# Kernel optimization log

Hardware: AMD Instinct MI355X
Metric: run time of the kernel (lower is better)

Reference implementation:

```python
import jax, jax.numpy as jnp
import numpy as np

B, T, C, H = 2, 2048, 1024, 16
D = C // H  # head_dim = 64

def setup_inputs() -> dict:
    key = jax.random.key(0)
    ks = jax.random.split(key, 5)
    x = jax.random.normal(ks[0], (B, T, C), dtype=jnp.float32)
    Wqkv = jax.random.normal(ks[1], (C, 3 * C), dtype=jnp.float32) * 0.02
    bqkv = jnp.zeros((3 * C,), dtype=jnp.float32)
    Wout = jax.random.normal(ks[2], (C, C), dtype=jnp.float32) * 0.02
    bout = jnp.zeros((C,), dtype=jnp.float32)
    return {"x": x, "Wqkv": Wqkv, "bqkv": bqkv, "Wout": Wout, "bout": bout}

def reference(x, Wqkv, bqkv, Wout, bout):
    Bb, Tt, Cc = x.shape
    qkv = x @ Wqkv + bqkv                       # [B,T,3C]
    qkv = qkv.reshape(Bb, Tt, 3, H, D)
    qkv = jnp.transpose(qkv, (2, 0, 3, 1, 4))   # [3,B,H,T,D]
    q, k, v = qkv[0], qkv[1], qkv[2]
    scale = 1.0 / np.sqrt(D).astype(np.float32)
    scores = jnp.einsum('bhqd,bhkd->bhqk', q, k) * scale  # [B,H,T,T]
    causal = jnp.tril(jnp.ones((Tt, Tt), dtype=bool))
    scores = jnp.where(causal[None, None, :, :], scores, jnp.float32(-jnp.inf))
    attn = jax.nn.softmax(scores, axis=-1)
    out = jnp.einsum('bhqk,bhkd->bhqd', attn, v)          # [B,H,T,D]
    out = jnp.transpose(out, (0, 2, 1, 3)).reshape(Bb, Tt, Cc)
    return out @ Wout + bout
```

## Files before the change

kernel.cpp:

```cpp
#include <hip/hip_runtime.h>

#define Bc 2
#define Tc 2048
#define Cc 1024
#define Hc 16
#define Dc 64
#define Mtot (Bc*Tc)
#define Kdim Cc
#define N1 (3*Cc)
#define N2 Cc

typedef __attribute__((ext_vector_type(8))) short short8;
typedef __attribute__((ext_vector_type(4))) float float4v;

__device__ __forceinline__ unsigned short f2bf(float f) {
  unsigned int u = __builtin_bit_cast(unsigned int, f);
  u += 0x7FFFu + ((u >> 16) & 1u);
  return (unsigned short)(u >> 16);
}

__device__ __forceinline__ unsigned int pk_bf16(float a, float b) {
#if __has_builtin(__builtin_amdgcn_cvt_pk_bf16_f32)
  typedef __attribute__((ext_vector_type(2))) __bf16 bf16x2;
  bf16x2 v = __builtin_amdgcn_cvt_pk_bf16_f32(a, b);
  return __builtin_bit_cast(unsigned int, v);
#else
  return (unsigned int)f2bf(a) | ((unsigned int)f2bf(b) << 16);
#endif
}

__device__ __forceinline__ void gl2lds16(const unsigned short* g, unsigned short* l) {
  __builtin_amdgcn_global_load_lds((const __attribute__((address_space(1))) void*)g,
                                   (__attribute__((address_space(3))) void*)l, 16, 0, 0);
}

__global__ __launch_bounds__(256) void k_prep(const float* __restrict__ wqkv,
                                              const float* __restrict__ wout,
                                              const float* __restrict__ x,
                                              unsigned short* __restrict__ wqkvT,
                                              unsigned short* __restrict__ woutT,
                                              unsigned short* __restrict__ xb) {
  const int bx = blockIdx.x;
  if (bx >= 128) {
    int idx = ((bx - 128) * 32 + blockIdx.y) * 256 + threadIdx.x;
    float4 v = ((const float4*)x)[idx];
    uint2 o;
    o.x = pk_bf16(v.x, v.y);
    o.y = pk_bf16(v.z, v.w);
    ((uint2*)xb)[idx] = o;
    return;
  }
  __shared__ float tile[32][33];
  const float* w;  unsigned short* wT;  int N, n0;
  if (bx < 96) { w = wqkv; wT = wqkvT; N = N1; n0 = bx * 32; }
  else         { w = wout; wT = woutT; N = N2; n0 = (bx - 96) * 32; }
  const int k0 = blockIdx.y * 32;
  int tx = threadIdx.x & 31, ty = threadIdx.x >> 5;
  for (int i = 0; i < 4; ++i)
    tile[ty + 8*i][tx] = w[(size_t)(k0 + ty + 8*i) * N + n0 + tx];
  __syncthreads();
  for (int i = 0; i < 4; ++i)
    wT[(size_t)(n0 + ty + 8*i) * Kdim + k0 + tx] = f2bf(tile[tx][ty + 8*i]);
}

__global__ __launch_bounds__(256) void k_gemm_qkv(const unsigned short* __restrict__ A,
                                                  const unsigned short* __restrict__ BT,
                                                  const float* __restrict__ bias,
                                                  unsigned short* __restrict__ qkv) {
  __shared__ alignas(16) unsigned short smem[64*136 + 64];
  unsigned short* As = smem;
  unsigned short* Bs = smem + 4096;
  const int m0 = blockIdx.y * 128, n0 = blockIdx.x * 128;
  const int tid = threadIdx.x;
  const int w = tid >> 6, lane = tid & 63;
  const int ln = lane & 15, qd = lane >> 4;
  const int wm = w >> 1, wn = w & 1;
  const int c0 = tid, c1 = tid + 256;
  const int row0 = c0 >> 2, ko0 = (c0 & 3) * 8;
  const int row1 = c1 >> 2, ko1 = (c1 & 3) * 8;
  const float4v zero4 = {0.f, 0.f, 0.f, 0.f};
  float4v acc[4][4];
  for (int i = 0; i < 4; ++i) for (int j = 0; j < 4; ++j) acc[i][j] = zero4;
  for (int kk = 0; kk < Kdim; kk += 32) {
    __syncthreads();
    gl2lds16(A  + (size_t)(m0 + row0) * Kdim + kk + ko0, As + c0 * 8);
    gl2lds16(A  + (size_t)(m0 + row1) * Kdim + kk + ko1, As + c1 * 8);
    gl2lds16(BT + (size_t)(n0 + row0) * Kdim + kk + ko0, Bs + c0 * 8);
    gl2lds16(BT + (size_t)(n0 + row1) * Kdim + kk + ko1, Bs + c1 * 8);
    __syncthreads();
    short8 af[4], bf[4];
    for (int i = 0; i < 4; ++i)
      af[i] = *(const short8*)(As + (wm*64 + i*16 + ln) * 32 + qd*8);
    for (int j = 0; j < 4; ++j)
      bf[j] = *(const short8*)(Bs + (wn*64 + j*16 + ln) * 32 + qd*8);
    for (int i = 0; i < 4; ++i)
      for (int j = 0; j < 4; ++j)
        acc[i][j] = __builtin_amdgcn_mfma_f32_16x16x32_bf16(af[i], bf[j], acc[i][j], 0, 0, 0);
  }
  const int s = n0 >> 10;
  if (s < 2) {
    const float scale = (s == 0) ? 0.125f : 1.0f;
    for (int i = 0; i < 4; ++i) {
      int mbase = m0 + wm*64 + i*16 + qd*4;
      for (int j = 0; j < 4; ++j) {
        int ncol = n0 + wn*64 + j*16 + ln;
        float bv = bias[ncol];
        int rem = ncol & 1023;
        int h = rem >> 6, d = rem & 63;
        for (int r = 0; r < 4; ++r) {
          int m = mbase + r;
          int b = m >> 11, t = m & 2047;
          float val = (acc[i][j][r] + bv) * scale;
          qkv[((((size_t)s*Bc + b)*Hc + h)*Tc + t)*Dc + d] = f2bf(val);
        }
      }
    }
  } else {
    unsigned short* vbase = qkv + (size_t)2*Bc*Hc*Tc*Dc;
    const int b = m0 >> 11, t0 = m0 & 2047;
    const int h0 = (n0 & 1023) >> 6;
    for (int p = 0; p < 2; ++p) {
      __syncthreads();
      if (wn == p) {
        for (int i = 0; i < 4; ++i) {
          int tl = wm*64 + i*16 + qd*4;
          for (int j = 0; j < 4; ++j) {
            int dl = j*16 + ln;
            float bv = bias[n0 + p*64 + dl];
            uint2 pk;
            pk.x = pk_bf16(acc[i][j][0] + bv, acc[i][j][1] + bv);
            pk.y = pk_bf16(acc[i][j][2] + bv, acc[i][j][3] + bv);
            *(uint2*)(smem + dl*136 + tl) = pk;
          }
        }
      }
      __syncthreads();
      for (int ii = 0; ii < 4; ++ii) {
        int idx = tid + 256*ii;
        int row = idx >> 4, c16 = idx & 15;
        int4 v = *(const int4*)(smem + row*136 + c16*8);
        *(int4*)(vbase + (((size_t)b*Hc + h0 + p)*Dc + row)*Tc + t0 + c16*8) = v;
      }
    }
  }
}

__global__ __launch_bounds__(256) void k_gemm_out(const unsigned short* __restrict__ A,
                                                  const unsigned short* __restrict__ BT,
                                                  const float* __restrict__ bias,
                                                  float* __restrict__ out) {
  __shared__ alignas(16) unsigned short As[64*32];
  __shared__ alignas(16) unsigned short Bs[128*32];
  const int m0 = blockIdx.y * 64, n0 = blockIdx.x * 128;
  const int tid = threadIdx.x;
  const int w = tid >> 6, lane = tid & 63;
  const int ln = lane & 15, qd = lane >> 4;
  const int wm = w >> 1, wn = w & 1;
  const int arow = tid >> 2, ako = (tid & 3) * 8;
  const int c0 = tid, c1 = tid + 256;
  const int brow0 = c0 >> 2, bko0 = (c0 & 3) * 8;
  const int brow1 = c1 >> 2, bko1 = (c1 & 3) * 8;
  const float4v zero4 = {0.f, 0.f, 0.f, 0.f};
  float4v acc[2][4];
  for (int i = 0; i < 2; ++i) for (int j = 0; j < 4; ++j) acc[i][j] = zero4;
  for (int kk = 0; kk < Kdim; kk += 32) {
    __syncthreads();
    gl2lds16(A  + (size_t)(m0 + arow)  * Kdim + kk + ako,  As + tid * 8);
    gl2lds16(BT + (size_t)(n0 + brow0) * Kdim + kk + bko0, Bs + c0 * 8);
    gl2lds16(BT + (size_t)(n0 + brow1) * Kdim + kk + bko1, Bs + c1 * 8);
    __syncthreads();
    short8 af[2], bf[4];
    for (int i = 0; i < 2; ++i)
      af[i] = *(const short8*)(As + (wm*32 + i*16 + ln) * 32 + qd*8);
    for (int j = 0; j < 4; ++j)
      bf[j] = *(const short8*)(Bs + (wn*64 + j*16 + ln) * 32 + qd*8);
    for (int i = 0; i < 2; ++i)
      for (int j = 0; j < 4; ++j)
        acc[i][j] = __builtin_amdgcn_mfma_f32_16x16x32_bf16(af[i], bf[j], acc[i][j], 0, 0, 0);
  }
  for (int i = 0; i < 2; ++i) {
    int mbase = m0 + wm*32 + i*16 + qd*4;
    for (int j = 0; j < 4; ++j) {
      int ncol = n0 + wn*64 + j*16 + ln;
      float bv = bias[ncol];
      for (int r = 0; r < 4; ++r)
        out[(size_t)(mbase + r) * N2 + ncol] = acc[i][j][r] + bv;
    }
  }
}

__device__ __forceinline__ void attn_substep(
    const unsigned short* __restrict__ Ks, const unsigned short* __restrict__ Vt,
    unsigned short* __restrict__ pw,
    const short8 qa0, const short8 qa1,
    float4v* o, float& l_part,
    int k0, int myq, bool mask, int ln, int qd)
{
  const float L2E = 1.44269504f;
  const float SH = 23.0831098f;
  const float4v zero4 = {0.f, 0.f, 0.f, 0.f};
  float4v s[4];
  for (int ki = 0; ki < 4; ++ki) {
    s[ki] = zero4;
    const unsigned short* kr = Ks + (ki*16 + ln)*72;
    short8 kf0 = *(const short8*)(kr + qd*8);
    short8 kf1 = *(const short8*)(kr + 32 + qd*8);
    s[ki] = __builtin_amdgcn_mfma_f32_16x16x32_bf16(kf0, qa0, s[ki], 0, 0, 0);
    s[ki] = __builtin_amdgcn_mfma_f32_16x16x32_bf16(kf1, qa1, s[ki], 0, 0, 0);
  }
  if (mask) {
    for (int ki = 0; ki < 4; ++ki) {
      int key = k0 + ki*16 + qd*4;
      for (int r = 0; r < 4; ++r)
        if (key + r > myq) s[ki][r] = -1e30f;
    }
  }
  float st = 0.f;
  for (int ki = 0; ki < 4; ++ki) {
    float p0 = exp2f(fmaf(s[ki][0], L2E, -SH));
    float p1 = exp2f(fmaf(s[ki][1], L2E, -SH));
    float p2 = exp2f(fmaf(s[ki][2], L2E, -SH));
    float p3 = exp2f(fmaf(s[ki][3], L2E, -SH));
    st += (p0 + p1) + (p2 + p3);
    uint2 pk2;
    pk2.x = pk_bf16(p0, p1);
    pk2.y = pk_bf16(p2, p3);
    *(uint2*)(pw + ln*72 + ki*16 + qd*4) = pk2;
  }
  l_part += st;
  short8 pb0 = *(const short8*)(pw + ln*72 + qd*8);
  short8 pb1 = *(const short8*)(pw + ln*72 + 32 + qd*8);
  for (int dt = 0; dt < 4; ++dt) {
    const unsigned short* vr = Vt + (dt*16 + ln)*72;
    short8 va0 = *(const short8*)(vr + qd*8);
    short8 va1 = *(const short8*)(vr + 32 + qd*8);
    o[dt] = __builtin_amdgcn_mfma_f32_16x16x32_bf16(va0, pb0, o[dt], 0, 0, 0);
    o[dt] = __builtin_amdgcn_mfma_f32_16x16x32_bf16(va1, pb1, o[dt], 0, 0, 0);
  }
}

__global__ __launch_bounds__(256) void k_attn(const unsigned short* __restrict__ qb,
                                              const unsigned short* __restrict__ kb,
                                              const unsigned short* __restrict__ vT,
                                              unsigned short* __restrict__ ob) {
  __shared__ alignas(16) unsigned short Ks[2][64*72];
  __shared__ alignas(16) unsigned short Vt[2][64*72];
  __shared__ alignas(16) unsigned short Ps[4][16*72];
  const int bh = blockIdx.x;
  const int pp = blockIdx.y;
  const int qtA = 31 - pp, qtB = pp;
  const int tid = threadIdx.x;
  const int w = tid >> 6, lane = tid & 63;
  const int ln = lane & 15, qd = lane >> 4;
  const size_t base = (size_t)bh * Tc * Dc;
  const int b = bh >> 4, h = bh & 15;
  const int srow = tid >> 3, scol = (tid & 7) * 8;
  const float4v zero4 = {0.f, 0.f, 0.f, 0.f};
  unsigned short* pw = Ps[w];

  const int myqA = qtA*64 + w*16 + ln;
  const int myqB = qtB*64 + w*16 + ln;
  const unsigned short* qrA = qb + base + (size_t)myqA * Dc;
  const unsigned short* qrB = qb + base + (size_t)myqB * Dc;
  short8 qaA0 = *(const short8*)(qrA + qd*8);
  short8 qaA1 = *(const short8*)(qrA + 32 + qd*8);
  short8 qaB0 = *(const short8*)(qrB + qd*8);
  short8 qaB1 = *(const short8*)(qrB + 32 + qd*8);
  float4v oA[4], oB[4];
  for (int dt = 0; dt < 4; ++dt) { oA[dt] = zero4; oB[dt] = zero4; }
  float lA = 0.f, lB = 0.f;

  {
    int4 k0v = *(const int4*)(kb + base + (size_t)srow * Dc + scol);
    int4 k1v = *(const int4*)(kb + base + (size_t)(srow + 32) * Dc + scol);
    int4 v0v = *(const int4*)(vT + base + (size_t)srow * Tc + scol);
    int4 v1v = *(const int4*)(vT + base + (size_t)(srow + 32) * Tc + scol);
    *(int4*)(Ks[0] + srow*72 + scol)      = k0v;
    *(int4*)(Ks[0] + (srow+32)*72 + scol) = k1v;
    *(int4*)(Vt[0] + srow*72 + scol)      = v0v;
    *(int4*)(Vt[0] + (srow+32)*72 + scol) = v1v;
  }
  __syncthreads();

  for (int kt = 0; kt <= qtA; ++kt) {
    const int cur = kt & 1;
    int4 rk0, rk1, rv0, rv1;
    if (kt < qtA) {
      const int k0n = (kt + 1) * 64;
      rk0 = *(const int4*)(kb + base + (size_t)(k0n + srow) * Dc + scol);
      rk1 = *(const int4*)(kb + base + (size_t)(k0n + srow + 32) * Dc + scol);
      rv0 = *(const int4*)(vT + base + (size_t)srow * Tc + k0n + scol);
      rv1 = *(const int4*)(vT + base + (size_t)(srow + 32) * Tc + k0n + scol);
    }
    attn_substep(Ks[cur], Vt[cur], pw, qaA0, qaA1, oA, lA, kt*64, myqA, kt == qtA, ln, qd);
    if (kt <= qtB)
      attn_substep(Ks[cur], Vt[cur], pw, qaB0, qaB1, oB, lB, kt*64, myqB, kt == qtB, ln, qd);
    if (kt < qtA) {
      const int nxt = cur ^ 1;
      *(int4*)(Ks[nxt] + srow*72 + scol)      = rk0;
      *(int4*)(Ks[nxt] + (srow+32)*72 + scol) = rk1;
      *(int4*)(Vt[nxt] + srow*72 + scol)      = rv0;
      *(int4*)(Vt[nxt] + (srow+32)*72 + scol) = rv1;
      __syncthreads();
    }
  }
  lA += __shfl_xor(lA, 16); lA += __shfl_xor(lA, 32);
  lB += __shfl_xor(lB, 16); lB += __shfl_xor(lB, 32);
  float invA = 1.0f / lA, invB = 1.0f / lB;
  for (int dt = 0; dt < 4; ++dt) {
    uint2 ovA, ovB;
    ovA.x = pk_bf16(oA[dt][0] * invA, oA[dt][1] * invA);
    ovA.y = pk_bf16(oA[dt][2] * invA, oA[dt][3] * invA);
    *(uint2*)(ob + (size_t)(b*Tc + myqA)*Cc + h*Dc + dt*16 + qd*4) = ovA;
    ovB.x = pk_bf16(oB[dt][0] * invB, oB[dt][1] * invB);
    ovB.y = pk_bf16(oB[dt][2] * invB, oB[dt][3] * invB);
    *(uint2*)(ob + (size_t)(b*Tc + myqB)*Cc + h*Dc + dt*16 + qd*4) = ovB;
  }
}

extern "C" void kernel_launch(void* const* d_in, const int* in_sizes, int n_in,
                              void* d_out, int out_size, void* d_ws, size_t ws_size,
                              hipStream_t stream) {
  const float* x    = (const float*)d_in[0];
  const float* Wqkv = (const float*)d_in[1];
  const float* bqkv = (const float*)d_in[2];
  const float* Wout = (const float*)d_in[3];
  const float* bout = (const float*)d_in[4];
  float* out = (float*)d_out;

  char* ws = (char*)d_ws;
  unsigned short* xb    = (unsigned short*)ws;
  unsigned short* wqkvT = (unsigned short*)(ws + 8388608);
  unsigned short* woutT = (unsigned short*)(ws + 14680064);
  unsigned short* qkvb  = (unsigned short*)(ws + 16777216);

  k_prep<<<dim3(256, 32), 256, 0, stream>>>(Wqkv, Wout, x, wqkvT, woutT, xb);
  k_gemm_qkv<<<dim3(N1/128, Mtot/128), 256, 0, stream>>>(xb, wqkvT, bqkv, qkvb);
  k_attn<<<dim3(32, 16), 256, 0, stream>>>(qkvb, qkvb + (size_t)Bc*Hc*Tc*Dc,
                                           qkvb + (size_t)2*Bc*Hc*Tc*Dc, xb);
  k_gemm_out<<<dim3(N2/128, Mtot/64), 256, 0, stream>>>(xb, woutT, bout, out);
}
```

Measured before the change: 198.4 us.

## Read K/V fragments directly from global memory and drop paired query tiles

The attention kernel no longer stages K and V tiles in double-buffered shared memory. Each wave now loads its MFMA operand fragments straight from global memory, relying on the cache for reuse across the four waves. The balanced pairing of a long and a short query tile per block is replaced by one query tile per block on a grid twice as large, with a launch-bounds occupancy hint added. This cuts shared-memory traffic and register pressure, but each wave issues redundant global loads, load latency is no longer hidden by prefetch, and the causal work per block is now uneven.

Result: slower. 295.4 us (+48.9%).

```diff
diff --git a/kernel.cpp b/kernel.cpp
--- a/kernel.cpp
+++ b/kernel.cpp
@@ -189,8 +189,8 @@
   }
 }
 
-__device__ __forceinline__ void attn_substep(
-    const unsigned short* __restrict__ Ks, const unsigned short* __restrict__ Vt,
+__device__ __forceinline__ void attn_substep_g(
+    const unsigned short* __restrict__ Kg, const unsigned short* __restrict__ Vg,
     unsigned short* __restrict__ pw,
     const short8 qa0, const short8 qa1,
     float4v* o, float& l_part,
@@ -198,15 +198,14 @@
 {
   const float L2E = 1.44269504f;
   const float SH = 23.0831098f;
-  const float4v zero4 = {0.f, 0.f, 0.f, 0.f};
   float4v s[4];
   for (int ki = 0; ki < 4; ++ki) {
-    s[ki] = zero4;
-    const unsigned short* kr = Ks + (ki*16 + ln)*72;
+    const unsigned short* kr = Kg + (size_t)(k0 + ki*16 + ln) * Dc;
     short8 kf0 = *(const short8*)(kr + qd*8);
     short8 kf1 = *(const short8*)(kr + 32 + qd*8);
-    s[ki] = __builtin_amdgcn_mfma_f32_16x16x32_bf16(kf0, qa0, s[ki], 0, 0, 0);
-    s[ki] = __builtin_amdgcn_mfma_f32_16x16x32_bf16(kf1, qa1, s[ki], 0, 0, 0);
+    float4v z = {0.f, 0.f, 0.f, 0.f};
+    z = __builtin_amdgcn_mfma_f32_16x16x32_bf16(kf0, qa0, z, 0, 0, 0);
+    s[ki] = __builtin_amdgcn_mfma_f32_16x16x32_bf16(kf1, qa1, z, 0, 0, 0);
   }
   if (mask) {
     for (int ki = 0; ki < 4; ++ki) {
@@ -231,7 +230,7 @@
   short8 pb0 = *(const short8*)(pw + ln*72 + qd*8);
   short8 pb1 = *(const short8*)(pw + ln*72 + 32 + qd*8);
   for (int dt = 0; dt < 4; ++dt) {
-    const unsigned short* vr = Vt + (dt*16 + ln)*72;
+    const unsigned short* vr = Vg + (size_t)(dt*16 + ln) * Tc + k0;
     short8 va0 = *(const short8*)(vr + qd*8);
     short8 va1 = *(const short8*)(vr + 32 + qd*8);
     o[dt] = __builtin_amdgcn_mfma_f32_16x16x32_bf16(va0, pb0, o[dt], 0, 0, 0);
@@ -239,82 +238,42 @@
   }
 }
 
-__global__ __launch_bounds__(256) void k_attn(const unsigned short* __restrict__ qb,
-                                              const unsigned short* __restrict__ kb,
-                                              const unsigned short* __restrict__ vT,
-                                              unsigned short* __restrict__ ob) {
-  __shared__ alignas(16) unsigned short Ks[2][64*72];
-  __shared__ alignas(16) unsigned short Vt[2][64*72];
+__global__ __launch_bounds__(256, 4) void k_attn(const unsigned short* __restrict__ qb,
+                                                 const unsigned short* __restrict__ kb,
+                                                 const unsigned short* __restrict__ vT,
+                                                 unsigned short* __restrict__ ob) {
   __shared__ alignas(16) unsigned short Ps[4][16*72];
   const int bh = blockIdx.x;
-  const int pp = blockIdx.y;
-  const int qtA = 31 - pp, qtB = pp;
+  const int qt = 31 - blockIdx.y;
   const int tid = threadIdx.x;
   const int w = tid >> 6, lane = tid & 63;
   const int ln = lane & 15, qd = lane >> 4;
   const size_t base = (size_t)bh * Tc * Dc;
   const int b = bh >> 4, h = bh & 15;
-  const int srow = tid >> 3, scol = (tid & 7) * 8;
   const float4v zero4 = {0.f, 0.f, 0.f, 0.f};
   unsigned short* pw = Ps[w];
 
-  const int myqA = qtA*64 + w*16 + ln;
-  const int myqB = qtB*64 + w*16 + ln;
-  const unsigned short* qrA = qb + base + (size_t)myqA * Dc;
-  const unsigned short* qrB = qb + base + (size_t)myqB * Dc;
-  short8 qaA0 = *(const short8*)(qrA + qd*8);
-  short8 qaA1 = *(const short8*)(qrA + 32 + qd*8);
-  short8 qaB0 = *(const short8*)(qrB + qd*8);
-  short8 qaB1 = *(const short8*)(qrB + 32 + qd*8);
-  float4v oA[4], oB[4];
-  for (int dt = 0; dt < 4; ++dt) { oA[dt] = zero4; oB[dt] = zero4; }
-  float lA = 0.f, lB = 0.f;
-
-  {
-    int4 k0v = *(const int4*)(kb + base + (size_t)srow * Dc + scol);
-    int4 k1v = *(const int4*)(kb + base + (size_t)(srow + 32) * Dc + scol);
-    int4 v0v = *(const int4*)(vT + base + (size_t)srow * Tc + scol);
-    int4 v1v = *(const int4*)(vT + base + (size_t)(srow + 32) * Tc + scol);
-    *(int4*)(Ks[0] + srow*72 + scol)      = k0v;
-    *(int4*)(Ks[0] + (srow+32)*72 + scol) = k1v;
-    *(int4*)(Vt[0] + srow*72 + scol)      = v0v;
-    *(int4*)(Vt[0] + (srow+32)*72 + scol) = v1v;
-  }
-  __syncthreads();
-
-  for (int kt = 0; kt <= qtA; ++kt) {
-    const int cur = kt & 1;
-    int4 rk0, rk1, rv0, rv1;
-    if (kt < qtA) {
-      const int k0n = (kt + 1) * 64;
-      rk0 = *(const int4*)(kb + base + (size_t)(k0n + srow) * Dc + scol);
-      rk1 = *(const int4*)(kb + base + (size_t)(k0n + srow + 32) * Dc + scol);
-      rv0 = *(const int4*)(vT + base + (size_t)srow * Tc + k0n + scol);
-      rv1 = *(const int4*)(vT + base + (size_t)(srow + 32) * Tc + k0n + scol);
-    }
-    attn_substep(Ks[cur], Vt[cur], pw, qaA0, qaA1, oA, lA, kt*64, myqA, kt == qtA, ln, qd);
-    if (kt <= qtB)
-      attn_substep(Ks[cur], Vt[cur], pw, qaB0, qaB1, oB, lB, kt*64, myqB, kt == qtB, ln, qd);
-    if (kt < qtA) {
-      const int nxt = cur ^ 1;
-      *(int4*)(Ks[nxt] + srow*72 + scol)      = rk0;
-      *(int4*)(Ks[nxt] + (srow+32)*72 + scol) = rk1;
-      *(int4*)(Vt[nxt] + srow*72 + scol)      = rv0;
-      *(int4*)(Vt[nxt] + (srow+32)*72 + scol) = rv1;
-      __syncthreads();
-    }
-  }
-  lA += __shfl_xor(lA, 16); lA += __shfl_xor(lA, 32);
-  lB += __shfl_xor(lB, 16); lB += __shfl_xor(lB, 32);
-  float invA = 1.0f / lA, invB = 1.0f / lB;
+  const int myq = qt*64 + w*16 + ln;
+  const unsigned short* qr = qb + base + (size_t)myq * Dc;
+  short8 qa0 = *(const short8*)(qr + qd*8);
+  short8 qa1 = *(const short8*)(qr + 32 + qd*8);
+  float4v o[4];
+  for (int dt = 0; dt < 4; ++dt) o[dt] = zero4;
+  float l = 0.f;
+  const unsigned short* Kg = kb + base;
+  const unsigned short* Vg = vT + base;
+
+  for (int kt = 0; kt <= qt; ++kt) {
+    __syncthreads();
+    attn_substep_g(Kg, Vg, pw, qa0, qa1, o, l, kt*64, myq, kt == qt, ln, qd);
+  }
+  l += __shfl_xor(l, 16); l += __shfl_xor(l, 32);
+  float inv = 1.0f / l;
   for (int dt = 0; dt < 4; ++dt) {
-    uint2 ovA, ovB;
-    ovA.x = pk_bf16(oA[dt][0] * invA, oA[dt][1] * invA);
-    ovA.y = pk_bf16(oA[dt][2] * invA, oA[dt][3] * invA);
-    *(uint2*)(ob + (size_t)(b*Tc + myqA)*Cc + h*Dc + dt*16 + qd*4) = ovA;
-    ovB.x = pk_bf16(oB[dt][0] * invB, oB[dt][1] * invB);
-    ovB.y = pk_bf16(oB[dt][2] * invB, oB[dt][3] * invB);
-    *(uint2*)(ob + (size_t)(b*Tc + myqB)*Cc + h*Dc + dt*16 + qd*4) = ovB;
+    uint2 ov;
+    ov.x = pk_bf16(o[dt][0] * inv, o[dt][1] * inv);
+    ov.y = pk_bf16(o[dt][2] * inv, o[dt][3] * inv);
+    *(uint2*)(ob + (size_t)(b*Tc + myq)*Cc + h*Dc + dt*16 + qd*4) = ov;
   }
 }
 
@@ -336,7 +295,7 @@
 
   k_prep<<<dim3(256, 32), 256, 0, stream>>>(Wqkv, Wout, x, wqkvT, woutT, xb);
   k_gemm_qkv<<<dim3(N1/128, Mtot/128), 256, 0, stream>>>(xb, wqkvT, bqkv, qkvb);
-  k_attn<<<dim3(32, 16), 256, 0, stream>>>(qkvb, qkvb + (size_t)Bc*Hc*Tc*Dc,
+  k_attn<<<dim3(32, 32), 256, 0, stream>>>(qkvb, qkvb + (size_t)Bc*Hc*Tc*Dc,
                                            qkvb + (size_t)2*Bc*Hc*Tc*Dc, xb);
   k_gemm_out<<<dim3(N2/128, Mtot/64), 256, 0, stream>>>(xb, woutT, bout, out);
 }
```
